# Performance work log

Hardware: AMD Instinct MI355X
Metric: run time of the kernel (lower is better)

The kernel has to match this reference:

```python
import jax, jax.numpy as jnp
import numpy as np
import math

B, H, S, D = 2, 16, 2048, 64

def setup_inputs() -> dict:
    key = jax.random.key(0)
    kq, kk, kv = jax.random.split(key, 3)
    return {
        "q": jax.random.normal(kq, (B, H, S, D), dtype=jnp.float32),
        "k": jax.random.normal(kk, (B, H, S, D), dtype=jnp.float32),
        "v": jax.random.normal(kv, (B, H, S, D), dtype=jnp.float32),
        "temp": jnp.ones((1,), dtype=jnp.float32),
    }

def reference(q, k, v, temp):
    dk = q.shape[-1]
    # scores: [B,H,S,S] = q @ k^T / (temp * sqrt(dk))
    scores = jnp.einsum("bhsd,bhtd->bhst", q, k) / (temp[0] * math.sqrt(dk))
    attention = jax.nn.softmax(scores, axis=-1)
    y = jnp.einsum("bhst,bhtd->bhsd", attention, v)
    return y
```

## Files before the change

kernel.cpp:

```cpp
#include <hip/hip_runtime.h>
#include <stdint.h>


typedef _Float16 f16;
typedef __attribute__((ext_vector_type(4))) _Float16 f16x4;
typedef __attribute__((ext_vector_type(8))) _Float16 f16x8;
typedef __attribute__((ext_vector_type(4))) float f32x4;

constexpr int Bc = 2, Hc = 16, Sc = 2048, Dc = 64;
constexpr size_t NE = (size_t)Bc * Hc * Sc * Dc;

__device__ inline void gld_lds16(const f16* g, f16* l) {
  __builtin_amdgcn_global_load_lds(
      (const __attribute__((address_space(1))) unsigned int*)g,
      (__attribute__((address_space(3))) unsigned int*)l, 16, 0, 0);
}

__global__ __launch_bounds__(256)
void prep(const float* __restrict__ kp, const float* __restrict__ vp,
          const float* __restrict__ temp,
          f16* __restrict__ kh, f16* __restrict__ vt) {
  const int tid = threadIdx.x;
  const int bh = blockIdx.x & 31;
  const int st = blockIdx.x >> 5;
  const float ksc = 1.44269504088896340736f / (temp[0] * 8.0f);

  const size_t base = (size_t)bh * Sc * Dc + (size_t)st * 64 * Dc;
  const float* kg = kp + base;
  f16* khg = kh + base;
#pragma unroll
  for (int i = 0; i < 4; ++i) {
    int f = tid + (i << 8);
    f32x4 a = *(const f32x4*)(kg + f * 4);
    *(f16x4*)(khg + f * 4) = (f16x4){(f16)(a.x * ksc), (f16)(a.y * ksc),
                                     (f16)(a.z * ksc), (f16)(a.w * ksc)};
  }
  const int sb = tid & 15, db = tid >> 4;
  const float* vg = vp + base;
  f32x4 r0 = *(const f32x4*)(vg + (4 * sb + 0) * Dc + 4 * db);
  f32x4 r1 = *(const f32x4*)(vg + (4 * sb + 1) * Dc + 4 * db);
  f32x4 r2 = *(const f32x4*)(vg + (4 * sb + 2) * Dc + 4 * db);
  f32x4 r3 = *(const f32x4*)(vg + (4 * sb + 3) * Dc + 4 * db);
  f16* vtg = vt + (size_t)bh * Dc * Sc + (size_t)st * 64 + 4 * sb;
  *(f16x4*)(vtg + (size_t)(4 * db + 0) * Sc) = (f16x4){(f16)r0.x, (f16)r1.x, (f16)r2.x, (f16)r3.x};
  *(f16x4*)(vtg + (size_t)(4 * db + 1) * Sc) = (f16x4){(f16)r0.y, (f16)r1.y, (f16)r2.y, (f16)r3.y};
  *(f16x4*)(vtg + (size_t)(4 * db + 2) * Sc) = (f16x4){(f16)r0.z, (f16)r1.z, (f16)r2.z, (f16)r3.z};
  *(f16x4*)(vtg + (size_t)(4 * db + 3) * Sc) = (f16x4){(f16)r0.w, (f16)r1.w, (f16)r2.w, (f16)r3.w};
}

__global__ __launch_bounds__(256, 3)
void fa10(const float* __restrict__ qp, const f16* __restrict__ kh,
          const f16* __restrict__ vt, float* __restrict__ out) {
  __shared__ __align__(16) char smem[33792];
  __shared__ float Lred[4][64];

  const int tid = threadIdx.x, lane = tid & 63, w = tid >> 6;
  const int lq = lane & 15, qd = lane >> 4;
  const int L = blockIdx.x;
  const int bh = L & 31;
  const int qt = L >> 5;

  const size_t base = (size_t)bh * Sc * Dc;

  f16* Kw = (f16*)smem + w * 2048;
  f16* Vw = (f16*)(smem + 16384) + w * 2048;

  const int oct = (lane & 7) ^ ((lane >> 3) & 7);
  const f16* kg0 = kh + base + (size_t)(16 * w + (lane >> 3)) * 64 + oct * 8;
  const f16* kg1 = kg0 + 8 * 64;
  const int vd = lane >> 1;
  const int vc = (lane & 1) ^ ((lane >> 3) & 1);
  const f16* vg0 = vt + (size_t)bh * Dc * Sc + (size_t)vd * Sc + 16 * w + vc * 8;
  const f16* vg1 = vg0 + (size_t)32 * Sc;

  auto stage = [&](int kt, int b) {
    gld_lds16(kg0 + (size_t)kt * 4096, Kw + b * 1024);
    gld_lds16(kg1 + (size_t)kt * 4096, Kw + b * 1024 + 512);
    gld_lds16(vg0 + kt * 64, Vw + b * 1024);
    gld_lds16(vg1 + kt * 64, Vw + b * 1024 + 512);
  };

  const int koff0 = lq * 64 + ((qd) ^ (lq & 7)) * 8;
  const int koff1 = lq * 64 + ((4 + qd) ^ (lq & 7)) * 8;
  int voff[4];
#pragma unroll
  for (int dt = 0; dt < 4; ++dt)
    voff[dt] = (16 * dt + lq) * 16 + (((qd >> 1) ^ ((lq >> 2) & 1)) << 3) +
               (qd & 1) * 4;

  const float* qg = qp + base + (size_t)qt * 64 * Dc;
  f16x8 Qf[4][2];
#pragma unroll
  for (int nt = 0; nt < 4; ++nt)
#pragma unroll
    for (int kc = 0; kc < 2; ++kc) {
      const float* p = qg + (16 * nt + lq) * Dc + 32 * kc + 8 * qd;
      f32x4 a = *(const f32x4*)p;
      f32x4 b = *(const f32x4*)(p + 4);
      auto p0 = __builtin_amdgcn_cvt_pkrtz(a.x, a.y);
      auto p1 = __builtin_amdgcn_cvt_pkrtz(a.z, a.w);
      auto p2 = __builtin_amdgcn_cvt_pkrtz(b.x, b.y);
      auto p3 = __builtin_amdgcn_cvt_pkrtz(b.z, b.w);
      f16x8 qf;
      ((decltype(p0)*)&qf)[0] = p0;
      ((decltype(p0)*)&qf)[1] = p1;
      ((decltype(p0)*)&qf)[2] = p2;
      ((decltype(p0)*)&qf)[3] = p3;
      Qf[nt][kc] = qf;
    }

  float z0 = 0.f, z1 = 0.f, z2 = 0.f, z3 = 0.f;
  asm volatile("" : "+v"(z0), "+v"(z1), "+v"(z2), "+v"(z3));
  const f32x4 Zc = (f32x4){z0, z1, z2, z3};

  f32x4 Oa[4][4];
  float ls[4];
#pragma unroll
  for (int nt = 0; nt < 4; ++nt) {
    ls[nt] = 0.f;
#pragma unroll
    for (int dt = 0; dt < 4; ++dt) Oa[nt][dt] = (f32x4){0.f, 0.f, 0.f, 0.f};
  }

  stage(0, 0);
  stage(1, 1);

#define FA_BODY(BUF, WN, STGKT)                                               \
  {                                                                           \
    asm volatile("s_waitcnt vmcnt(" WN ")" ::: "memory");                     \
    const f16* KB = Kw + (BUF) * 1024;                                        \
    const f16* VB = Vw + (BUF) * 1024;                                        \
    f16x8 K0 = *(const f16x8*)(KB + koff0);                                   \
    f16x8 K1 = *(const f16x8*)(KB + koff1);                                   \
    f16x4 Vf[4];                                                              \
    _Pragma("unroll")                                                         \
    for (int dt = 0; dt < 4; ++dt) Vf[dt] = *(const f16x4*)(VB + voff[dt]);   \
    asm volatile("s_waitcnt lgkmcnt(0)" ::: "memory");                        \
    if ((STGKT) < 32) stage((STGKT), (BUF));                                  \
    f32x4 St[4];                                                              \
    _Pragma("unroll")                                                         \
    for (int nt = 0; nt < 4; ++nt) {                                          \
      f32x4 a = __builtin_amdgcn_mfma_f32_16x16x32_f16(K0, Qf[nt][0], Zc, 0, 0, 0); \
      a = __builtin_amdgcn_mfma_f32_16x16x32_f16(K1, Qf[nt][1], a, 0, 0, 0);  \
      St[nt] = a;                                                             \
    }                                                                         \
    f16x4 Pf[4];                                                              \
    _Pragma("unroll")                                                         \
    for (int nt = 0; nt < 4; ++nt) {                                          \
      float e0 = __builtin_amdgcn_exp2f(St[nt].x);                            \
      float e1 = __builtin_amdgcn_exp2f(St[nt].y);                            \
      float e2 = __builtin_amdgcn_exp2f(St[nt].z);                            \
      float e3 = __builtin_amdgcn_exp2f(St[nt].w);                            \
      ls[nt] += (e0 + e1) + (e2 + e3);                                        \
      auto lo = __builtin_amdgcn_cvt_pkrtz(e0, e1);                           \
      auto hi = __builtin_amdgcn_cvt_pkrtz(e2, e3);                           \
      f16x4 p;                                                                \
      ((decltype(lo)*)&p)[0] = lo;                                            \
      ((decltype(lo)*)&p)[1] = hi;                                            \
      Pf[nt] = p;                                                             \
    }                                                                         \
    _Pragma("unroll")                                                         \
    for (int nt = 0; nt < 4; ++nt)                                            \
      _Pragma("unroll")                                                       \
      for (int dt = 0; dt < 4; ++dt)                                          \
        Oa[nt][dt] = __builtin_amdgcn_mfma_f32_16x16x16f16(Pf[nt], Vf[dt],    \
                                                           Oa[nt][dt], 0, 0, 0); \
  }

#pragma unroll 1
  for (int kt2 = 0; kt2 < 15; ++kt2) {
    FA_BODY(0, "4", 2 * kt2 + 2)
    FA_BODY(1, "4", 2 * kt2 + 3)
  }
  FA_BODY(0, "4", 32)
  FA_BODY(1, "0", 32)

#undef FA_BODY

#pragma unroll
  for (int nt = 0; nt < 4; ++nt) {
    float l = ls[nt];
    l += __shfl_xor(l, 16, 64);
    l += __shfl_xor(l, 32, 64);
    ls[nt] = l;
  }
  __syncthreads();
  if (qd == 0) {
#pragma unroll
    for (int nt = 0; nt < 4; ++nt) Lred[w][16 * nt + lq] = ls[nt];
  }
  float* OsA = (float*)smem;
  float* OsB = (float*)(smem + 16896);
  float* Os = (w & 2) ? OsB : OsA;
  if (!(w & 1)) {
#pragma unroll
    for (int nt = 0; nt < 4; ++nt)
#pragma unroll
      for (int dt = 0; dt < 4; ++dt)
#pragma unroll
        for (int r = 0; r < 4; ++r)
          Os[(16 * nt + 4 * qd + r) * 66 + 16 * dt + lq] = Oa[nt][dt][r];
  }
  __syncthreads();
  if (w & 1) {
#pragma unroll
    for (int nt = 0; nt < 4; ++nt)
#pragma unroll
      for (int dt = 0; dt < 4; ++dt)
#pragma unroll
        for (int r = 0; r < 4; ++r)
          Os[(16 * nt + 4 * qd + r) * 66 + 16 * dt + lq] += Oa[nt][dt][r];
  }
  __syncthreads();

  float* og = out + base + (size_t)qt * 64 * Dc;
#pragma unroll
  for (int r = 0; r < 16; ++r) {
    int row = 16 * w + r;
    float l = Lred[0][row] + Lred[1][row] + Lred[2][row] + Lred[3][row];
    float vo = OsA[row * 66 + lane] + OsB[row * 66 + lane];
    og[(size_t)row * Dc + lane] = vo / l;
  }
}

extern "C" void kernel_launch(void* const* d_in, const int* in_sizes, int n_in,
                              void* d_out, int out_size, void* d_ws, size_t ws_size,
                              hipStream_t stream) {
  const float* q    = (const float*)d_in[0];
  const float* k    = (const float*)d_in[1];
  const float* v    = (const float*)d_in[2];
  const float* temp = (const float*)d_in[3];
  float* out = (float*)d_out;

  f16* kh = (f16*)d_ws;
  f16* vt = kh + NE;

  prep<<<dim3(Bc * Hc * (Sc / 64)), dim3(256), 0, stream>>>(k, v, temp, kh, vt);
  fa10<<<dim3(Bc * Hc * (Sc / 64)), dim3(256), 0, stream>>>(q, kh, vt, out);
}
```

Measured before the change: 142.7 us.

## Triple-buffer K/V tiles in LDS and prefetch next K fragments into registers

Moves from double to triple buffering of the per-wave K/V LDS tiles, raising shared memory from about 33 KB to 48 KB. K fragments for the next tile are loaded into alternating register sets during the current iteration, and the V loads and next global stage are placed after the QK MFMAs. The loop is unrolled by six to rotate the buffers. The aim is to hide LDS and global-load latency behind MFMA work. The cost is higher LDS use, which may reduce occupancy below three blocks per CU, plus extra registers.

After: 348.3 us. 144% more time.

```diff
diff --git a/kernel.cpp b/kernel.cpp
--- a/kernel.cpp
+++ b/kernel.cpp
@@ -49,9 +49,9 @@
 }
 
 __global__ __launch_bounds__(256, 3)
-void fa10(const float* __restrict__ qp, const f16* __restrict__ kh,
+void fa11(const float* __restrict__ qp, const f16* __restrict__ kh,
           const f16* __restrict__ vt, float* __restrict__ out) {
-  __shared__ __align__(16) char smem[33792];
+  __shared__ __align__(16) char smem[49152];
   __shared__ float Lred[4][64];
 
   const int tid = threadIdx.x, lane = tid & 63, w = tid >> 6;
@@ -62,8 +62,8 @@
 
   const size_t base = (size_t)bh * Sc * Dc;
 
-  f16* Kw = (f16*)smem + w * 2048;
-  f16* Vw = (f16*)(smem + 16384) + w * 2048;
+  f16* Kw = (f16*)smem + w * 3072;
+  f16* Vw = (f16*)(smem + 24576) + w * 3072;
 
   const int oct = (lane & 7) ^ ((lane >> 3) & 7);
   const f16* kg0 = kh + base + (size_t)(16 * w + (lane >> 3)) * 64 + oct * 8;
@@ -124,26 +124,26 @@
 
   stage(0, 0);
   stage(1, 1);
-
-#define FA_BODY(BUF, WN, STGKT)                                               \
+  asm volatile("s_waitcnt vmcnt(4)" ::: "memory");
+  f16x8 KA0 = *(const f16x8*)(Kw + koff0);
+  f16x8 KA1 = *(const f16x8*)(Kw + koff1);
+  f16x8 KB0, KB1;
+
+#define FA_BODY(BUF, NBUF, SBUF, STGKT, WN, KC0, KC1, KP0, KP1, DO_PF)        \
   {                                                                           \
-    asm volatile("s_waitcnt vmcnt(" WN ")" ::: "memory");                     \
-    const f16* KB = Kw + (BUF) * 1024;                                        \
-    const f16* VB = Vw + (BUF) * 1024;                                        \
-    f16x8 K0 = *(const f16x8*)(KB + koff0);                                   \
-    f16x8 K1 = *(const f16x8*)(KB + koff1);                                   \
-    f16x4 Vf[4];                                                              \
-    _Pragma("unroll")                                                         \
-    for (int dt = 0; dt < 4; ++dt) Vf[dt] = *(const f16x4*)(VB + voff[dt]);   \
-    asm volatile("s_waitcnt lgkmcnt(0)" ::: "memory");                        \
-    if ((STGKT) < 32) stage((STGKT), (BUF));                                  \
     f32x4 St[4];                                                              \
     _Pragma("unroll")                                                         \
     for (int nt = 0; nt < 4; ++nt) {                                          \
-      f32x4 a = __builtin_amdgcn_mfma_f32_16x16x32_f16(K0, Qf[nt][0], Zc, 0, 0, 0); \
-      a = __builtin_amdgcn_mfma_f32_16x16x32_f16(K1, Qf[nt][1], a, 0, 0, 0);  \
+      f32x4 a = __builtin_amdgcn_mfma_f32_16x16x32_f16(KC0, Qf[nt][0], Zc, 0, 0, 0); \
+      a = __builtin_amdgcn_mfma_f32_16x16x32_f16(KC1, Qf[nt][1], a, 0, 0, 0); \
       St[nt] = a;                                                             \
     }                                                                         \
+    const f16* VB = Vw + (BUF) * 1024;                                        \
+    f16x4 Vf[4];                                                              \
+    _Pragma("unroll")                                                         \
+    for (int dt = 0; dt < 4; ++dt) Vf[dt] = *(const f16x4*)(VB + voff[dt]);   \
+    asm volatile("s_waitcnt lgkmcnt(4)" ::: "memory");                        \
+    if ((STGKT) < 32) stage((STGKT), (SBUF));                                 \
     f16x4 Pf[4];                                                              \
     _Pragma("unroll")                                                         \
     for (int nt = 0; nt < 4; ++nt) {                                          \
@@ -159,6 +159,12 @@
       ((decltype(lo)*)&p)[1] = hi;                                            \
       Pf[nt] = p;                                                             \
     }                                                                         \
+    asm volatile("s_waitcnt vmcnt(" WN ")" ::: "memory");                     \
+    if (DO_PF) {                                                              \
+      const f16* KBn = Kw + (NBUF) * 1024;                                    \
+      KP0 = *(const f16x8*)(KBn + koff0);                                     \
+      KP1 = *(const f16x8*)(KBn + koff1);                                     \
+    }                                                                         \
     _Pragma("unroll")                                                         \
     for (int nt = 0; nt < 4; ++nt)                                            \
       _Pragma("unroll")                                                       \
@@ -168,12 +174,17 @@
   }
 
 #pragma unroll 1
-  for (int kt2 = 0; kt2 < 15; ++kt2) {
-    FA_BODY(0, "4", 2 * kt2 + 2)
-    FA_BODY(1, "4", 2 * kt2 + 3)
-  }
-  FA_BODY(0, "4", 32)
-  FA_BODY(1, "0", 32)
+  for (int kt6 = 0; kt6 < 5; ++kt6) {
+    const int k0 = 6 * kt6;
+    FA_BODY(0, 1, 2, k0 + 2, "4", KA0, KA1, KB0, KB1, 1)
+    FA_BODY(1, 2, 0, k0 + 3, "4", KB0, KB1, KA0, KA1, 1)
+    FA_BODY(2, 0, 1, k0 + 4, "4", KA0, KA1, KB0, KB1, 1)
+    FA_BODY(0, 1, 2, k0 + 5, "4", KB0, KB1, KA0, KA1, 1)
+    FA_BODY(1, 2, 0, k0 + 6, "4", KA0, KA1, KB0, KB1, 1)
+    FA_BODY(2, 0, 1, k0 + 7, "4", KB0, KB1, KA0, KA1, 1)
+  }
+  FA_BODY(0, 1, 2, 32, "0", KA0, KA1, KB0, KB1, 1)
+  FA_BODY(1, 2, 0, 32, "0", KB0, KB1, KA0, KA1, 0)
 
 #undef FA_BODY
 
@@ -236,5 +247,5 @@
   f16* vt = kh + NE;
 
   prep<<<dim3(Bc * Hc * (Sc / 64)), dim3(256), 0, stream>>>(k, v, temp, kh, vt);
-  fa10<<<dim3(Bc * Hc * (Sc / 64)), dim3(256), 0, stream>>>(q, kh, vt, out);
-}
+  fa11<<<dim3(Bc * Hc * (Sc / 64)), dim3(256), 0, stream>>>(q, kh, vt, out);
+}
```
